# Optimization experiments

Hardware: AMD Instinct MI355X
Metric: run time of the kernel (lower is better)

Reference implementation:

```python
import jax, jax.numpy as jnp
import numpy as np

EMB, HID, OUT = 512, 512, 512

def setup_inputs() -> dict:
    key = jax.random.key(0)
    ks = jax.random.split(key, 7)
    s = 1.0 / np.sqrt(EMB + HID)
    so = 1.0 / np.sqrt(2 * HID)
    return {
        "input_seq": jax.random.normal(ks[0], (32, 512, EMB), dtype=jnp.float32),
        "W_f": jax.random.uniform(ks[1], (EMB + HID, HID), jnp.float32, -s, s),
        "b_f": jax.random.uniform(ks[2], (HID,), jnp.float32, -s, s),
        "W_b": jax.random.uniform(ks[3], (EMB + HID, HID), jnp.float32, -s, s),
        "b_b": jax.random.uniform(ks[4], (HID,), jnp.float32, -s, s),
        "W_o": jax.random.uniform(ks[5], (2 * HID, OUT), jnp.float32, -so, so),
        "b_o": jax.random.uniform(ks[6], (OUT,), jnp.float32, -so, so),
    }

def _rnn_scan(xs, W, b, h0, reverse):
    # split W into input and hidden parts to avoid per-step concat
    Wx, Wh = W[:EMB], W[EMB:]
    def step(h, x_t):
        h_new = jnp.tanh(x_t @ Wx + h @ Wh + b)
        return h_new, h_new
    _, hs = jax.lax.scan(step, h0, xs, reverse=reverse)  # hs: [S, B, H]
    return hs

def reference(input_seq, W_f, b_f, W_b, b_b, W_o, b_o):
    B = input_seq.shape[0]
    xs = jnp.swapaxes(input_seq, 0, 1)  # [S, B, E]
    h0 = jnp.zeros((B, HID), input_seq.dtype)
    hs_f = _rnn_scan(xs, W_f, b_f, h0, reverse=False)   # [S, B, H]
    hs_b = _rnn_scan(xs, W_b, b_b, h0, reverse=True)    # [S, B, H], already time-aligned
    bi = jnp.concatenate([hs_f, hs_b], axis=-1)          # [S, B, 2H]
    out = bi @ W_o + b_o                                 # [S, B, O]
    return jnp.swapaxes(out, 0, 1)                       # [B, S, O]
```

## Files before the change

### kernel.cpp

```cpp
#include <hip/hip_runtime.h>
#include <hip/hip_fp16.h>
#include <stdint.h>

#define SEQ 512
#define HIDN 512

typedef _Float16 h2_t __attribute__((ext_vector_type(2)));
typedef _Float16 h8_t __attribute__((ext_vector_type(8)));
typedef float f4_t __attribute__((ext_vector_type(4)));

__device__ __forceinline__ float fdot2f(uint32_t a, uint32_t b, float c) {
#if __has_builtin(__builtin_amdgcn_fdot2)
  return __builtin_amdgcn_fdot2(__builtin_bit_cast(h2_t, a),
                                __builtin_bit_cast(h2_t, b), c, false);
#else
  h2_t ah = __builtin_bit_cast(h2_t, a);
  h2_t bh = __builtin_bit_cast(h2_t, b);
  return c + (float)ah.x * (float)bh.x + (float)ah.y * (float)bh.y;
#endif
}

__global__ void k_cvt(const float4* __restrict__ src, __half2* __restrict__ dst, int n4) {
  int i = blockIdx.x * blockDim.x + threadIdx.x;
  if (i < n4) {
    float4 v = src[i];
    dst[2 * i]     = __floats2half2_rn(v.x, v.y);
    dst[2 * i + 1] = __floats2half2_rn(v.z, v.w);
  }
}

__global__ void k_transpose_cvt(const float* __restrict__ src, __half* __restrict__ dst,
                                int R, int C) {
  __shared__ float tile[32][33];
  int tx = threadIdx.x, ty = threadIdx.y;
  int c0 = blockIdx.x * 32, r0 = blockIdx.y * 32;
#pragma unroll
  for (int i = 0; i < 4; ++i)
    tile[ty + i * 8][tx] = src[(size_t)(r0 + ty + i * 8) * C + c0 + tx];
  __syncthreads();
#pragma unroll
  for (int i = 0; i < 4; ++i)
    dst[(size_t)(c0 + ty + i * 8) * R + r0 + tx] = __float2half(tile[tx][ty + i * 8]);
}

__global__ __launch_bounds__(256, 2) void k_gemm(
    const __half* __restrict__ A, const __half* __restrict__ Bt,
    const float* __restrict__ bias, float* __restrict__ C,
    int M, int N, int K) {
  __shared__ __align__(16) __half As[128 * 32];
  __shared__ __align__(16) __half Bs[128 * 32];
  const int tid = threadIdx.x;
  const int m0 = blockIdx.x * 128;
  const int n0 = blockIdx.y * 128;
  const int w = tid >> 6;
  const int lane = tid & 63;
  const int wm = (w >> 1) * 64;
  const int wn = (w & 1) * 64;
  const int fr = lane & 15;
  const int q = lane >> 4;
  const int lr = tid >> 2;
  const int lc = tid & 3;
  f4_t acc[4][4];
#pragma unroll
  for (int i = 0; i < 4; ++i)
#pragma unroll
    for (int jj = 0; jj < 4; ++jj) acc[i][jj] = (f4_t)(0.f);

  for (int kk = 0; kk < K; kk += 32) {
    *(uint4*)&As[lr * 32 + lc * 8]        = *(const uint4*)&A[(size_t)(m0 + lr) * K + kk + lc * 8];
    *(uint4*)&As[(64 + lr) * 32 + lc * 8] = *(const uint4*)&A[(size_t)(m0 + 64 + lr) * K + kk + lc * 8];
    *(uint4*)&Bs[lr * 32 + lc * 8]        = *(const uint4*)&Bt[(size_t)(n0 + lr) * K + kk + lc * 8];
    *(uint4*)&Bs[(64 + lr) * 32 + lc * 8] = *(const uint4*)&Bt[(size_t)(n0 + 64 + lr) * K + kk + lc * 8];
    __syncthreads();
    h8_t af[4], bf[4];
#pragma unroll
    for (int i = 0; i < 4; ++i) {
      af[i] = *(const h8_t*)&As[(wm + i * 16 + fr) * 32 + q * 8];
      bf[i] = *(const h8_t*)&Bs[(wn + i * 16 + fr) * 32 + q * 8];
    }
#pragma unroll
    for (int i = 0; i < 4; ++i)
#pragma unroll
      for (int jj = 0; jj < 4; ++jj)
        acc[i][jj] = __builtin_amdgcn_mfma_f32_16x16x32_f16(af[i], bf[jj], acc[i][jj], 0, 0, 0);
    __syncthreads();
  }
#pragma unroll
  for (int i = 0; i < 4; ++i) {
    const int row0 = m0 + wm + i * 16 + q * 4;
#pragma unroll
    for (int jj = 0; jj < 4; ++jj) {
      const int col = n0 + wn + jj * 16 + fr;
      const float bv = bias[col];
#pragma unroll
      for (int r = 0; r < 4; ++r)
        C[(size_t)(row0 + r) * N + col] = acc[i][jj][r] + bv;
    }
  }
}

__global__ __launch_bounds__(512, 2) void k_rnn(
    const __half* __restrict__ WhT_f, const __half* __restrict__ WhT_b,
    const float* __restrict__ A_f, const float* __restrict__ A_b,
    __half* __restrict__ bi) {
  __shared__ uint32_t ldsw[56 * HIDN];
  __shared__ __align__(16) __half hbuf[2][HIDN];
  const int j = threadIdx.x;
  const int d = blockIdx.x & 1;
  const int b = blockIdx.x >> 1;
  const __half* WhT = d ? WhT_b : WhT_f;
  const float* A = (d ? A_b : A_f) + (size_t)b * SEQ * HIDN;
  __half* birow = bi + (size_t)b * SEQ * 1024 + d * HIDN + j;

  const uint4* wrow = (const uint4*)(WhT + (size_t)j * HIDN);
  uint4 wv[50];
#pragma unroll
  for (int i = 0; i < 50; ++i) wv[i] = wrow[i];
  const uint32_t* wrow32 = (const uint32_t*)wrow;
#pragma unroll
  for (int p = 0; p < 56; ++p) ldsw[p * HIDN + j] = wrow32[200 + p];
  hbuf[0][j] = __float2half(0.f);
  __syncthreads();

  const int tstep = d ? -1 : 1;
  int t = d ? (SEQ - 1) : 0;
  float a_next = A[(size_t)t * HIDN + j];
  int cur = 0;
  for (int s = 0; s < SEQ; ++s) {
    float a_cur = a_next;
    int tn = t + tstep;
    tn = tn < 0 ? 0 : (tn > SEQ - 1 ? SEQ - 1 : tn);
    a_next = A[(size_t)tn * HIDN + j];
    const uint4* hp = (const uint4*)hbuf[cur];
    float acc0 = 0.f, acc1 = 0.f, acc2 = 0.f, acc3 = 0.f;
#pragma unroll
    for (int i = 0; i < 50; ++i) {
      uint4 hv = hp[i];
      acc0 = fdot2f(hv.x, wv[i].x, acc0);
      acc1 = fdot2f(hv.y, wv[i].y, acc1);
      acc2 = fdot2f(hv.z, wv[i].z, acc2);
      acc3 = fdot2f(hv.w, wv[i].w, acc3);
    }
#pragma unroll
    for (int p4 = 0; p4 < 14; ++p4) {
      uint4 hv = hp[50 + p4];
      acc0 = fdot2f(hv.x, ldsw[(p4 * 4 + 0) * HIDN + j], acc0);
      acc1 = fdot2f(hv.y, ldsw[(p4 * 4 + 1) * HIDN + j], acc1);
      acc2 = fdot2f(hv.z, ldsw[(p4 * 4 + 2) * HIDN + j], acc2);
      acc3 = fdot2f(hv.w, ldsw[(p4 * 4 + 3) * HIDN + j], acc3);
    }
    float p = a_cur + ((acc0 + acc1) + (acc2 + acc3));
    float ap = fabsf(p);
    float e = __expf(2.f * ap);
    float th = 1.f - 2.f * __builtin_amdgcn_rcpf(e + 1.f);
    float h = copysignf(th, p);
    __half hh = __float2half(h);
    hbuf[cur ^ 1][j] = hh;
    birow[(size_t)t * 1024] = hh;
    cur ^= 1;
    t += tstep;
    __syncthreads();
  }
}

extern "C" void kernel_launch(void* const* d_in, const int* in_sizes, int n_in,
                              void* d_out, int out_size, void* d_ws, size_t ws_size,
                              hipStream_t stream) {
  const float* input_seq = (const float*)d_in[0];
  const float* W_f = (const float*)d_in[1];
  const float* b_f = (const float*)d_in[2];
  const float* W_b = (const float*)d_in[3];
  const float* b_b = (const float*)d_in[4];
  const float* W_o = (const float*)d_in[5];
  const float* b_o = (const float*)d_in[6];
  float* out = (float*)d_out;

  char* ws = (char*)d_ws;
  __half* Xh    = (__half*)(ws);
  float*  A_f   = (float*)(ws + 16777216);
  float*  A_b   = (float*)(ws + 50331648);
  __half* bi    = (__half*)(ws + 83886080);
  __half* WxT_f = (__half*)(ws + 117440512);
  __half* WxT_b = (__half*)(ws + 117964800);
  __half* WhT_f = (__half*)(ws + 118489088);
  __half* WhT_b = (__half*)(ws + 119013376);
  __half* WoT   = (__half*)(ws + 119537664);

  k_cvt<<<8192, 256, 0, stream>>>((const float4*)input_seq, (__half2*)Xh, 2097152);
  dim3 tb(32, 8);
  k_transpose_cvt<<<dim3(16, 16), tb, 0, stream>>>(W_f,          WxT_f, 512, 512);
  k_transpose_cvt<<<dim3(16, 16), tb, 0, stream>>>(W_f + 262144, WhT_f, 512, 512);
  k_transpose_cvt<<<dim3(16, 16), tb, 0, stream>>>(W_b,          WxT_b, 512, 512);
  k_transpose_cvt<<<dim3(16, 16), tb, 0, stream>>>(W_b + 262144, WhT_b, 512, 512);
  k_transpose_cvt<<<dim3(16, 32), tb, 0, stream>>>(W_o,          WoT, 1024, 512);

  k_gemm<<<dim3(128, 4), 256, 0, stream>>>(Xh, WxT_f, b_f, A_f, 16384, 512, 512);
  k_gemm<<<dim3(128, 4), 256, 0, stream>>>(Xh, WxT_b, b_b, A_b, 16384, 512, 512);

  k_rnn<<<64, 512, 0, stream>>>(WhT_f, WhT_b, A_f, A_b, bi);

  k_gemm<<<dim3(128, 4), 256, 0, stream>>>(bi, WoT, b_o, out, 16384, 512, 1024);
}
```

Baseline: 1.086 ms.

## Split recurrent dot product across two thread halves with LDS reduction

The RNN kernel now launches 1024 threads per block instead of 512. Each hidden unit's 512-long recurrent dot product is split between two threads, one per half of the K dimension. Each thread keeps 23 weight vectors in registers and 9 in LDS, then the two partial sums are combined through a shared-memory buffer. This halves the serial per-step work on the latency-bound recurrence, at the cost of an extra barrier per step, more LDS use, and tanh being computed redundantly in both halves.

```diff
diff --git a/kernel.cpp b/kernel.cpp
--- a/kernel.cpp
+++ b/kernel.cpp
@@ -99,42 +99,44 @@
   }
 }
 
-__global__ __launch_bounds__(512, 2) void k_rnn(
+__global__ __launch_bounds__(1024) void k_rnn(
     const __half* __restrict__ WhT_f, const __half* __restrict__ WhT_b,
     const float* __restrict__ A_f, const float* __restrict__ A_b,
     __half* __restrict__ bi) {
-  __shared__ uint32_t ldsw[56 * HIDN];
+  __shared__ __align__(16) uint4 ldsw4[9 * 1024];
   __shared__ __align__(16) __half hbuf[2][HIDN];
-  const int j = threadIdx.x;
+  __shared__ float psum[2][HIDN];
+  const int t = threadIdx.x;
+  const int j = t & 511;
+  const int half = t >> 9;
   const int d = blockIdx.x & 1;
   const int b = blockIdx.x >> 1;
   const __half* WhT = d ? WhT_b : WhT_f;
   const float* A = (d ? A_b : A_f) + (size_t)b * SEQ * HIDN;
   __half* birow = bi + (size_t)b * SEQ * 1024 + d * HIDN + j;
 
-  const uint4* wrow = (const uint4*)(WhT + (size_t)j * HIDN);
-  uint4 wv[50];
-#pragma unroll
-  for (int i = 0; i < 50; ++i) wv[i] = wrow[i];
-  const uint32_t* wrow32 = (const uint32_t*)wrow;
-#pragma unroll
-  for (int p = 0; p < 56; ++p) ldsw[p * HIDN + j] = wrow32[200 + p];
-  hbuf[0][j] = __float2half(0.f);
+  const uint4* wrow4 = (const uint4*)(WhT + (size_t)j * HIDN);
+  uint4 wv[23];
+#pragma unroll
+  for (int i = 0; i < 23; ++i) wv[i] = wrow4[half * 32 + i];
+#pragma unroll
+  for (int p = 0; p < 9; ++p) ldsw4[p * 1024 + t] = wrow4[half * 32 + 23 + p];
+  if (half == 0) hbuf[0][j] = __float2half(0.f);
   __syncthreads();
 
   const int tstep = d ? -1 : 1;
-  int t = d ? (SEQ - 1) : 0;
-  float a_next = A[(size_t)t * HIDN + j];
+  int tt = d ? (SEQ - 1) : 0;
+  float a_next = A[(size_t)tt * HIDN + j];
   int cur = 0;
   for (int s = 0; s < SEQ; ++s) {
     float a_cur = a_next;
-    int tn = t + tstep;
+    int tn = tt + tstep;
     tn = tn < 0 ? 0 : (tn > SEQ - 1 ? SEQ - 1 : tn);
     a_next = A[(size_t)tn * HIDN + j];
-    const uint4* hp = (const uint4*)hbuf[cur];
+    const uint4* hp = (const uint4*)hbuf[cur] + half * 32;
     float acc0 = 0.f, acc1 = 0.f, acc2 = 0.f, acc3 = 0.f;
 #pragma unroll
-    for (int i = 0; i < 50; ++i) {
+    for (int i = 0; i < 23; ++i) {
       uint4 hv = hp[i];
       acc0 = fdot2f(hv.x, wv[i].x, acc0);
       acc1 = fdot2f(hv.y, wv[i].y, acc1);
@@ -142,23 +144,26 @@
       acc3 = fdot2f(hv.w, wv[i].w, acc3);
     }
 #pragma unroll
-    for (int p4 = 0; p4 < 14; ++p4) {
-      uint4 hv = hp[50 + p4];
-      acc0 = fdot2f(hv.x, ldsw[(p4 * 4 + 0) * HIDN + j], acc0);
-      acc1 = fdot2f(hv.y, ldsw[(p4 * 4 + 1) * HIDN + j], acc1);
-      acc2 = fdot2f(hv.z, ldsw[(p4 * 4 + 2) * HIDN + j], acc2);
-      acc3 = fdot2f(hv.w, ldsw[(p4 * 4 + 3) * HIDN + j], acc3);
-    }
-    float p = a_cur + ((acc0 + acc1) + (acc2 + acc3));
+    for (int p = 0; p < 9; ++p) {
+      uint4 hv = hp[23 + p];
+      uint4 lw = ldsw4[p * 1024 + t];
+      acc0 = fdot2f(hv.x, lw.x, acc0);
+      acc1 = fdot2f(hv.y, lw.y, acc1);
+      acc2 = fdot2f(hv.z, lw.z, acc2);
+      acc3 = fdot2f(hv.w, lw.w, acc3);
+    }
+    psum[half][j] = (acc0 + acc1) + (acc2 + acc3);
+    __syncthreads();
+    float p = psum[0][j] + psum[1][j] + a_cur;
     float ap = fabsf(p);
     float e = __expf(2.f * ap);
     float th = 1.f - 2.f * __builtin_amdgcn_rcpf(e + 1.f);
     float h = copysignf(th, p);
     __half hh = __float2half(h);
     hbuf[cur ^ 1][j] = hh;
-    birow[(size_t)t * 1024] = hh;
+    if (half == 0) birow[(size_t)tt * 1024] = hh;
     cur ^= 1;
-    t += tstep;
+    tt += tstep;
     __syncthreads();
   }
 }
@@ -197,7 +202,7 @@
   k_gemm<<<dim3(128, 4), 256, 0, stream>>>(Xh, WxT_f, b_f, A_f, 16384, 512, 512);
   k_gemm<<<dim3(128, 4), 256, 0, stream>>>(Xh, WxT_b, b_b, A_b, 16384, 512, 512);
 
-  k_rnn<<<64, 512, 0, stream>>>(WhT_f, WhT_b, A_f, A_b, bi);
+  k_rnn<<<64, 1024, 0, stream>>>(WhT_f, WhT_b, A_f, A_b, bi);
 
   k_gemm<<<dim3(128, 4), 256, 0, stream>>>(bi, WoT, b_o, out, 16384, 512, 1024);
 }
```

New measurement: 998.5 us. -8.1%, faster.
